# Optimization experiments

Measured on AMD Instinct MI355X. Metric: run time of the kernel, lower is better.

## Reference

```python
import jax, jax.numpy as jnp
import numpy as np

IMG_SIZE = 256
NUM_ANGLES = 360
NUM_DET = 363  # ceil(sqrt(2) * IMG_SIZE)


def setup_inputs() -> dict:
    key = jax.random.key(0)
    sinogram = jax.random.normal(key, (2, 1, NUM_ANGLES, NUM_DET), dtype=jnp.float32)
    return {"sinogram": sinogram}


def _fbp(sinogram):
    B, C, A, D = sinogram.shape
    H = W = IMG_SIZE

    # ---- ramp filter in frequency domain (filter_type='ramp') ----
    freq = jnp.fft.fftfreq(D).astype(jnp.float32)          # (D,)
    filt = 2.0 * jnp.abs(freq)
    sino_fft = jnp.fft.fft(sinogram, axis=-1)
    filtered = jnp.fft.ifft(sino_fft * filt, axis=-1).real.astype(sinogram.dtype)  # (B,C,A,D)

    # ---- backprojection geometry ----
    angles = jnp.linspace(0.0, np.pi * (1.0 - 1.0 / A), A).astype(jnp.float32)  # (A,)
    coords = jnp.linspace(-1.0, 1.0, H).astype(jnp.float32)
    y_grid, x_grid = jnp.meshgrid(coords, coords, indexing='ij')  # (H,W) each

    cos_t = jnp.cos(angles)[:, None, None]  # (A,1,1)
    sin_t = jnp.sin(angles)[:, None, None]
    t = x_grid[None] * cos_t + y_grid[None] * sin_t          # (A,H,W)

    scale = (H - 1) / 2.0 * np.sqrt(2.0) / ((D - 1) / 2.0)
    t_norm = t / scale                                        # normalized grid x in [-1,1]-ish

    # grid_sample, mode='bilinear', padding_mode='zeros', align_corners=True
    # x-coordinate maps to detector index: u = (t_norm + 1)/2 * (D-1)
    u = (t_norm + 1.0) * 0.5 * (D - 1)                        # (A,H,W)
    u0 = jnp.floor(u)
    w1 = u - u0                                               # frac weight for right neighbor
    w0 = 1.0 - w1
    i0 = u0.astype(jnp.int32)
    i1 = i0 + 1
    valid0 = ((i0 >= 0) & (i0 < D)).astype(sinogram.dtype)
    valid1 = ((i1 >= 0) & (i1 < D)).astype(sinogram.dtype)
    i0c = jnp.clip(i0, 0, D - 1)
    i1c = jnp.clip(i1, 0, D - 1)

    HW = H * W
    idx0 = jnp.broadcast_to(i0c.reshape(1, 1, A, HW), (B, C, A, HW))
    idx1 = jnp.broadcast_to(i1c.reshape(1, 1, A, HW), (B, C, A, HW))
    v0 = jnp.take_along_axis(filtered, idx0, axis=-1)         # (B,C,A,HW)
    v1 = jnp.take_along_axis(filtered, idx1, axis=-1)

    w0m = (w0 * valid0).reshape(1, 1, A, HW)
    w1m = (w1 * valid1).reshape(1, 1, A, HW)
    contrib = v0 * w0m + v1 * w1m                             # (B,C,A,HW)

    recon = contrib.sum(axis=2).reshape(B, C, H, W)
    return recon * (np.pi / A)


def reference(sinogram):
    return _fbp(sinogram)
```

## Files before the change

### kernel.cpp

```cpp
#include <hip/hip_runtime.h>
#include <math.h>

#define IMG 256
#define NA  360
#define ND  363
#define NB  2
#define KMAX 181
#define ST  544
#define PAD 76

__global__ __launch_bounds__(384) void fbp_conv(const float* __restrict__ sino,
                                                float* __restrict__ filt) {
    __shared__ float ht[2 * ND - 1];
    const int row = blockIdx.x;
    const int t = threadIdx.x;

    for (int i = t; i < 2 * ND - 1; i += 384) {
        int n  = i - (ND - 1);
        int an = n < 0 ? -n : n;
        float v;
        if (an == 0) {
            v = (float)(KMAX * (KMAX + 1) / 2);
        } else {
            int m1 = (KMAX * an) % ND;
            int m2 = ((KMAX + 1) * an) % ND;
            float c1 = cospif(2.f * (float)m1 / (float)ND);
            float c2 = cospif(2.f * (float)m2 / (float)ND);
            float s  = sinpif((float)an / (float)ND);
            v = (182.f * c1 - 181.f * c2 - 1.f) / (4.f * s * s);
        }
        ht[i] = v * (4.f / ((float)ND * (float)ND));
    }
    __syncthreads();

    const float* __restrict__ srow = sino + (size_t)row * ND;
    float* __restrict__ orow = filt + (size_t)row * ST;

    if (t < ND) {
        float acc0 = 0.f, acc1 = 0.f;
        int x = t;
#pragma unroll 8
        for (int m = ND - 1; m >= 1; m -= 2) {
            float h0 = ht[x];
            float h1 = ht[x + 1];
            acc0 = fmaf(srow[m],     h0, acc0);
            acc1 = fmaf(srow[m - 1], h1, acc1);
            x += 2;
        }
        acc0 = fmaf(srow[0], ht[t + (ND - 1)], acc0 + acc1);
        orow[PAD + t] = acc0;
    }
    if (t < PAD) orow[t] = 0.f;
    if (t >= PAD && t < PAD + (ST - PAD - ND)) orow[PAD + ND + (t - PAD)] = 0.f;
}

__global__ __launch_bounds__(256, 8) void fbp_backproj(const float* __restrict__ filt,
                                                       float* __restrict__ out,
                                                       float K, float U0p) {
    __shared__ float2 tab[NA];
    __shared__ float  part[256];
    const int t = threadIdx.x;

    const int blk  = blockIdx.x;
    const int img  = blk >> 10;
    const int iy   = (blk >> 2) & 255;
    const int jx0  = (blk & 3) * 64;
    const int lane = t & 63;
    const int wv   = t >> 6;

    const float xg = -1.f + 2.f * (float)(jx0 + lane) / 255.f;
    const float yg = -1.f + 2.f * (float)iy / 255.f;

    for (int a = t; a < NA; a += 256) {
        float ang = (float)M_PI * (float)a / (float)NA;
        float s, c;
        sincosf(ang, &s, &c);
        tab[a] = make_float2(c * K, fmaf(yg, s * K, U0p));
    }
    __syncthreads();

    const float* __restrict__ base = filt + (size_t)img * NA * ST;
    float acc = 0.f;
    const int a0 = wv * (NA / 4);

#pragma unroll 6
    for (int a = a0; a < a0 + NA / 4; ++a) {
        float2 cs = tab[a];
        float u  = fmaf(xg, cs.x, cs.y);
        float uf = floorf(u);
        int   i0 = (int)uf;
        float w  = u - uf;
        const float* rowp = base + a * ST;
        float2 tp = *(const float2*)(rowp + i0);
        acc = fmaf(w, tp.y - tp.x, acc + tp.x);
    }

    part[t] = acc;
    __syncthreads();

    if (t < 64) {
        float s = part[t] + part[t + 64] + part[t + 128] + part[t + 192];
        out[img * 65536 + iy * 256 + jx0 + t] = s * ((float)M_PI / (float)NA);
    }
}

extern "C" void kernel_launch(void* const* d_in, const int* in_sizes, int n_in,
                              void* d_out, int out_size, void* d_ws, size_t ws_size,
                              hipStream_t stream) {
    const float* sino = (const float*)d_in[0];
    float* out = (float*)d_out;
    float* filt = (float*)d_ws;

    const double scale = (double)(IMG - 1) / 2.0 * sqrt(2.0) / ((double)(ND - 1) / 2.0);
    const float  K   = (float)(0.5 * (double)(ND - 1) / scale);
    const float  U0p = 0.5f * (float)(ND - 1) + (float)PAD;

    fbp_conv<<<NB * NA, 384, 0, stream>>>(sino, filt);
    fbp_backproj<<<2048, 256, 0, stream>>>(filt, out, K, U0p);
}
```

Before: 87.28 us.

## Register-block ramp convolution two outputs per thread, pack angle pairs in backprojection

The convolution kernel now handles two sinogram rows per block, and each thread computes two adjacent filtered outputs. It reads filter taps as float2 so every sinogram load feeds two FMAs, which halves per-output shared and global loads and halves the block count. The backprojection angle table is packed as float4 pairs, so each LDS read serves two angles and the loop is unrolled over angle pairs. The cost is more register pressure and more complex indexing in the convolution loop.

```diff
diff --git a/kernel.cpp b/kernel.cpp
--- a/kernel.cpp
+++ b/kernel.cpp
@@ -11,53 +11,75 @@
 
 __global__ __launch_bounds__(384) void fbp_conv(const float* __restrict__ sino,
                                                 float* __restrict__ filt) {
-    __shared__ float ht[2 * ND - 1];
-    const int row = blockIdx.x;
+    __shared__ float ht[726];
     const int t = threadIdx.x;
 
-    for (int i = t; i < 2 * ND - 1; i += 384) {
-        int n  = i - (ND - 1);
-        int an = n < 0 ? -n : n;
-        float v;
-        if (an == 0) {
-            v = (float)(KMAX * (KMAX + 1) / 2);
-        } else {
-            int m1 = (KMAX * an) % ND;
-            int m2 = ((KMAX + 1) * an) % ND;
-            float c1 = cospif(2.f * (float)m1 / (float)ND);
-            float c2 = cospif(2.f * (float)m2 / (float)ND);
-            float s  = sinpif((float)an / (float)ND);
-            v = (182.f * c1 - 181.f * c2 - 1.f) / (4.f * s * s);
+    for (int i = t; i < 726; i += 384) {
+        float v = 0.f;
+        if (i <= 724) {
+            int n  = i - 362;
+            int an = n < 0 ? -n : n;
+            if (an == 0) {
+                v = (float)(KMAX * (KMAX + 1) / 2);
+            } else {
+                int m1 = (KMAX * an) % ND;
+                int m2 = ((KMAX + 1) * an) % ND;
+                float c1 = cospif(2.f * (float)m1 / (float)ND);
+                float c2 = cospif(2.f * (float)m2 / (float)ND);
+                float s  = sinpif((float)an / (float)ND);
+                v = (182.f * c1 - 181.f * c2 - 1.f) / (4.f * s * s);
+            }
+            v *= 4.f / ((float)ND * (float)ND);
         }
-        ht[i] = v * (4.f / ((float)ND * (float)ND));
+        ht[i] = v;
     }
     __syncthreads();
 
+    const int r   = t / 192;
+    const int tt  = t - r * 192;
+    const int row = 2 * blockIdx.x + r;
     const float* __restrict__ srow = sino + (size_t)row * ND;
     float* __restrict__ orow = filt + (size_t)row * ST;
 
-    if (t < ND) {
+    if (tt < 182) {
+        const float2* ht2 = (const float2*)ht;
         float acc0 = 0.f, acc1 = 0.f;
-        int x = t;
-#pragma unroll 8
-        for (int m = ND - 1; m >= 1; m -= 2) {
-            float h0 = ht[x];
-            float h1 = ht[x + 1];
-            acc0 = fmaf(srow[m],     h0, acc0);
-            acc1 = fmaf(srow[m - 1], h1, acc1);
-            x += 2;
+        float2 p0 = ht2[tt];
+#pragma unroll 5
+        for (int c = 0; c < 90; ++c) {
+            float2 p1 = ht2[tt + 2 * c + 1];
+            float2 p2 = ht2[tt + 2 * c + 2];
+            float s0 = srow[362 - 4 * c];
+            float s1 = srow[361 - 4 * c];
+            float s2 = srow[360 - 4 * c];
+            float s3 = srow[359 - 4 * c];
+            acc0 = fmaf(s0, p0.x, acc0);  acc1 = fmaf(s0, p0.y, acc1);
+            acc0 = fmaf(s1, p0.y, acc0);  acc1 = fmaf(s1, p1.x, acc1);
+            acc0 = fmaf(s2, p1.x, acc0);  acc1 = fmaf(s2, p1.y, acc1);
+            acc0 = fmaf(s3, p1.y, acc0);  acc1 = fmaf(s3, p2.x, acc1);
+            p0 = p2;
         }
-        acc0 = fmaf(srow[0], ht[t + (ND - 1)], acc0 + acc1);
-        orow[PAD + t] = acc0;
+        {
+            float2 q1 = ht2[tt + 181];
+            float s2m = srow[2], s1m = srow[1], s0m = srow[0];
+            acc0 = fmaf(s2m, p0.x, acc0);  acc1 = fmaf(s2m, p0.y, acc1);
+            acc0 = fmaf(s1m, p0.y, acc0);  acc1 = fmaf(s1m, q1.x, acc1);
+            acc0 = fmaf(s0m, q1.x, acc0);  acc1 = fmaf(s0m, q1.y, acc1);
+        }
+        if (tt < 181) {
+            *(float2*)(orow + PAD + 2 * tt) = make_float2(acc0, acc1);
+        } else {
+            orow[PAD + 362] = acc0;
+        }
     }
-    if (t < PAD) orow[t] = 0.f;
-    if (t >= PAD && t < PAD + (ST - PAD - ND)) orow[PAD + ND + (t - PAD)] = 0.f;
+    for (int i = tt; i < PAD; i += 192) orow[i] = 0.f;
+    for (int i = tt; i < ST - (PAD + ND); i += 192) orow[PAD + ND + i] = 0.f;
 }
 
 __global__ __launch_bounds__(256, 8) void fbp_backproj(const float* __restrict__ filt,
                                                        float* __restrict__ out,
                                                        float K, float U0p) {
-    __shared__ float2 tab[NA];
+    __shared__ float4 tab4[NA / 2];
     __shared__ float  part[256];
     const int t = threadIdx.x;
 
@@ -71,28 +93,37 @@
     const float xg = -1.f + 2.f * (float)(jx0 + lane) / 255.f;
     const float yg = -1.f + 2.f * (float)iy / 255.f;
 
-    for (int a = t; a < NA; a += 256) {
-        float ang = (float)M_PI * (float)a / (float)NA;
-        float s, c;
-        sincosf(ang, &s, &c);
-        tab[a] = make_float2(c * K, fmaf(yg, s * K, U0p));
+    for (int p = t; p < NA / 2; p += 256) {
+        float a0 = (float)M_PI * (float)(2 * p)     / (float)NA;
+        float a1 = (float)M_PI * (float)(2 * p + 1) / (float)NA;
+        float s0, c0, s1, c1;
+        sincosf(a0, &s0, &c0);
+        sincosf(a1, &s1, &c1);
+        tab4[p] = make_float4(c0 * K, fmaf(yg, s0 * K, U0p),
+                              c1 * K, fmaf(yg, s1 * K, U0p));
     }
     __syncthreads();
 
     const float* __restrict__ base = filt + (size_t)img * NA * ST;
     float acc = 0.f;
-    const int a0 = wv * (NA / 4);
+    const int p0 = wv * 45;
 
-#pragma unroll 6
-    for (int a = a0; a < a0 + NA / 4; ++a) {
-        float2 cs = tab[a];
-        float u  = fmaf(xg, cs.x, cs.y);
+#pragma unroll 5
+    for (int p = p0; p < p0 + 45; ++p) {
+        float4 cy = tab4[p];
+        const float* rowp = base + (2 * p) * ST;
+        float u  = fmaf(xg, cy.x, cy.y);
         float uf = floorf(u);
         int   i0 = (int)uf;
         float w  = u - uf;
-        const float* rowp = base + a * ST;
         float2 tp = *(const float2*)(rowp + i0);
         acc = fmaf(w, tp.y - tp.x, acc + tp.x);
+        float u2  = fmaf(xg, cy.z, cy.w);
+        float uf2 = floorf(u2);
+        int   i2  = (int)uf2;
+        float w2  = u2 - uf2;
+        float2 tq = *(const float2*)(rowp + ST + i2);
+        acc = fmaf(w2, tq.y - tq.x, acc + tq.x);
     }
 
     part[t] = acc;
@@ -115,6 +146,6 @@
     const float  K   = (float)(0.5 * (double)(ND - 1) / scale);
     const float  U0p = 0.5f * (float)(ND - 1) + (float)PAD;
 
-    fbp_conv<<<NB * NA, 384, 0, stream>>>(sino, filt);
+    fbp_conv<<<NB * NA / 2, 384, 0, stream>>>(sino, filt);
     fbp_backproj<<<2048, 256, 0, stream>>>(filt, out, K, U0p);
 }
```

Measured after the change: 85.79 us. Within noise of the previous version (-1.7%).
